# Performance work log

Measured on AMD Instinct MI355X. Metric: run time of the kernel, lower is better.

## Reference

```python
import math
import jax, jax.numpy as jnp
import numpy as np

B, T, T_P, C, H = 4, 2048, 256, 768, 12
HD = C // H


def setup_inputs() -> dict:
    key = jax.random.key(0)
    k1, k2, k3, k4 = jax.random.split(key, 4)
    x = jax.random.normal(k1, (B, T, C), dtype=jnp.float32)
    prefix = jax.random.normal(k2, (B, T_P, C), dtype=jnp.float32)
    # torch nn.Linear weight layout: (out_features, in_features)
    W_qkv = jax.random.normal(k3, (3 * C, C), dtype=jnp.float32) * (1.0 / math.sqrt(C))
    W_out = jax.random.normal(k4, (C, C), dtype=jnp.float32) * (1.0 / math.sqrt(C))
    return {"x": x, "prefix": prefix, "W_qkv": W_qkv, "W_out": W_out}


def _mac_causal_mask(t_p: int, t: int) -> jnp.ndarray:
    total = t_p + t
    mask = jnp.zeros((total, total), dtype=bool)
    mask = mask.at[:t_p, t_p:].set(True)  # h tokens blocked from x tokens
    causal = jnp.triu(jnp.ones((t, t), dtype=bool), k=1)  # causal within x block
    return mask.at[t_p:, t_p:].set(causal)


def reference(x, prefix, W_qkv, W_out):
    b, t, c = x.shape
    t_p = prefix.shape[1]
    t_all = t_p + t
    x_full = jnp.concatenate([prefix, x], axis=1)          # (B, T_all, C)
    qkv = x_full @ W_qkv.T                                  # (B, T_all, 3C)
    q, k, v = jnp.split(qkv, 3, axis=-1)
    # (B, H, T_all, HD)
    q = q.reshape(b, t_all, H, HD).transpose(0, 2, 1, 3)
    k = k.reshape(b, t_all, H, HD).transpose(0, 2, 1, 3)
    v = v.reshape(b, t_all, H, HD).transpose(0, 2, 1, 3)
    scale = 1.0 / math.sqrt(HD)
    att = jnp.einsum('bhqd,bhkd->bhqk', q, k) * scale       # (B, H, T_all, T_all)
    mask = _mac_causal_mask(t_p, t)
    att = jnp.where(mask[None, None], -jnp.inf, att)
    att = jax.nn.softmax(att, axis=-1)                      # dropout = identity (eval)
    out = jnp.einsum('bhqk,bhkd->bhqd', att, v)             # (B, H, T_all, HD)
    out = out.transpose(0, 2, 1, 3).reshape(b, t_all, c)
    out = out @ W_out.T
    return out[:, t_p:, :]                                  # only x portion (B, T, C)
```

## Files before the change

### kernel.cpp

```cpp
#include <hip/hip_runtime.h>

constexpr int Bn   = 4;
constexpr int Tn   = 2048;
constexpr int TPn  = 256;
constexpr int TALLn = 2304;
constexpr int Cn   = 768;
constexpr int Hn   = 12;
constexpr int HDn  = 64;

typedef __bf16 bf16x4 __attribute__((ext_vector_type(4)));
typedef __bf16 bf16x8 __attribute__((ext_vector_type(8)));
typedef float  f32x4  __attribute__((ext_vector_type(4)));
typedef unsigned u32x4 __attribute__((ext_vector_type(4)));

__device__ __forceinline__ unsigned short f2bf(float f) {
    unsigned int x = __float_as_uint(f);
    x += 0x7fffu + ((x >> 16) & 1u);
    return (unsigned short)(x >> 16);
}

__device__ __forceinline__ unsigned cvt_pk_bf16(float a, float b) {
    unsigned r;
    asm("v_cvt_pk_bf16_f32 %0, %1, %2" : "=v"(r) : "v"(a), "v"(b));
    return r;
}

#define ASYNC16(gsrc, ldst)                                                           \
    __builtin_amdgcn_global_load_lds((__attribute__((address_space(1))) void*)(gsrc), \
                                     (__attribute__((address_space(3))) void*)(ldst), \
                                     16, 0, 0)

__global__ __launch_bounds__(256) void k_build_xfull(
        const float* __restrict__ x, const float* __restrict__ pre,
        unsigned short* __restrict__ xf) {
    int idx = blockIdx.x * 256 + threadIdx.x;
    int row = idx / (Cn / 4);
    int c   = (idx - row * (Cn / 4)) * 4;
    int b = row / TALLn, tt = row - b * TALLn;
    const float* src = (tt < TPn) ? pre + ((size_t)b * TPn + tt) * Cn + c
                                  : x   + ((size_t)b * Tn + (tt - TPn)) * Cn + c;
    float4 f = *reinterpret_cast<const float4*>(src);
    ushort4 o = { f2bf(f.x), f2bf(f.y), f2bf(f.z), f2bf(f.w) };
    *reinterpret_cast<ushort4*>(xf + (size_t)row * Cn + c) = o;
}

__global__ __launch_bounds__(256) void k_cast(
        const float* __restrict__ in, unsigned short* __restrict__ out) {
    int idx = (blockIdx.x * 256 + threadIdx.x) * 4;
    float4 f = *reinterpret_cast<const float4*>(in + idx);
    ushort4 o = { f2bf(f.x), f2bf(f.y), f2bf(f.z), f2bf(f.w) };
    *reinterpret_cast<ushort4*>(out + idx) = o;
}

__global__ __launch_bounds__(256) void k_qkv_gemm(
        const unsigned short* __restrict__ A, const unsigned short* __restrict__ W,
        unsigned short* __restrict__ Qb, unsigned short* __restrict__ Kb,
        unsigned short* __restrict__ Vt) {
    __shared__ __align__(16) unsigned short smem[16384];
    unsigned short* As = smem;
    unsigned short* Bs = smem + 8192;
    const int tid  = threadIdx.x;
    const int wave = tid >> 6;
    const int lane = tid & 63;
    const int g = lane >> 4, l16 = lane & 15;
    const int m0 = blockIdx.x * 128, n0 = blockIdx.y * 128;
    const int wr = wave >> 1, wc = wave & 1;

    f32x4 acc[4][4] = {};

    for (int k0 = 0; k0 < Cn; k0 += 64) {
        #pragma unroll
        for (int inst = 0; inst < 4; ++inst) {
            const int li = inst * 256 + tid;
            const int row = li >> 3, slot = li & 7;
            const int ch = slot ^ (row & 7);
            ASYNC16(A + (size_t)(m0 + row) * Cn + k0 + ch * 8,
                    &As[(inst * 256 + wave * 64) * 8]);
            ASYNC16(W + (size_t)(n0 + row) * Cn + k0 + ch * 8,
                    &Bs[(inst * 256 + wave * 64) * 8]);
        }
        __syncthreads();
        #pragma unroll
        for (int kk = 0; kk < 2; ++kk) {
            bf16x8 af[4], bfv[4];
            #pragma unroll
            for (int mt = 0; mt < 4; ++mt) {
                const int row = wr * 64 + mt * 16 + l16;
                const int slot = (kk * 4 + g) ^ (row & 7);
                af[mt] = *reinterpret_cast<const bf16x8*>(&As[row * 64 + slot * 8]);
            }
            #pragma unroll
            for (int nt = 0; nt < 4; ++nt) {
                const int row = wc * 64 + nt * 16 + l16;
                const int slot = (kk * 4 + g) ^ (row & 7);
                bfv[nt] = *reinterpret_cast<const bf16x8*>(&Bs[row * 64 + slot * 8]);
            }
            #pragma unroll
            for (int mt = 0; mt < 4; ++mt)
                #pragma unroll
                for (int nt = 0; nt < 4; ++nt)
                    acc[mt][nt] = __builtin_amdgcn_mfma_f32_16x16x32_bf16(
                            af[mt], bfv[nt], acc[mt][nt], 0, 0, 0);
        }
        __syncthreads();
    }

    const int b   = m0 / TALLn;
    const int t0  = m0 - b * TALLn;
    const int sel = n0 / Cn;
    const int hn0 = n0 - sel * Cn;
    constexpr float SCQ = 0.18033688011112042f;

    if (sel == 2) {
        #pragma unroll
        for (int mt = 0; mt < 4; ++mt)
            #pragma unroll
            for (int nt = 0; nt < 4; ++nt)
                #pragma unroll
                for (int r = 0; r < 4; ++r) {
                    const int t  = wr * 64 + mt * 16 + g * 4 + r;
                    const int hn = wc * 64 + nt * 16 + l16;
                    smem[hn * 128 + (((t >> 3) ^ (hn & 7)) << 3) + (t & 7)] =
                            f2bf(acc[mt][nt][r]);
                }
        __syncthreads();
        #pragma unroll
        for (int j = 0; j < 8; ++j) {
            const int u  = tid + 256 * j;
            const int hn = u >> 4, tc = u & 15;
            bf16x8 v = *reinterpret_cast<const bf16x8*>(
                    &smem[hn * 128 + ((tc ^ (hn & 7)) << 3)]);
            const int hh = (hn0 + hn) >> 6;
            const int dd = hn & 63;
            *reinterpret_cast<bf16x8*>(
                    &Vt[(((size_t)b * Hn + hh) * HDn + dd) * TALLn + t0 + tc * 8]) = v;
        }
    } else {
        #pragma unroll
        for (int mt = 0; mt < 4; ++mt)
            #pragma unroll
            for (int nt = 0; nt < 4; ++nt)
                #pragma unroll
                for (int r = 0; r < 4; ++r) {
                    const int t  = t0 + wr * 64 + mt * 16 + g * 4 + r;
                    const int hn = hn0 + wc * 64 + nt * 16 + l16;
                    const int h = hn >> 6, d = hn & 63;
                    if (sel == 0)
                        Qb[(((size_t)b * Hn + h) * TALLn + t) * HDn + d] =
                                f2bf(acc[mt][nt][r] * SCQ);
                    else
                        Kb[(((size_t)b * Hn + h) * TALLn + t) * HDn + d] =
                                f2bf(acc[mt][nt][r]);
                }
    }
}

__global__ __launch_bounds__(256) void k_attn(
        const unsigned short* __restrict__ Qb, const unsigned short* __restrict__ Kb,
        const unsigned short* __restrict__ Vt, unsigned short* __restrict__ Ob) {
    __shared__ __align__(16) unsigned short Ks[2][4096];
    __shared__ __align__(16) unsigned short Vs[2][4096];
    const int tid  = threadIdx.x;
    const int wq   = tid >> 6;
    const int lane = tid & 63;
    const int l16  = lane & 15;
    const int g    = lane >> 4;

    const int fb = blockIdx.x;
    const int j  = fb >> 3;
    const int bh = 6 * (fb & 7) + (j >> 4);
    const int pi = j & 15;
    const size_t kv = (size_t)bh * TALLn * HDn;

    int koff[4][2];
    #pragma unroll
    for (int band = 0; band < 4; ++band)
        #pragma unroll
        for (int ks = 0; ks < 2; ++ks)
            koff[band][ks] = (band * 16 + l16) * 64 + (((ks * 4 + g) ^ (l16 & 7)) << 3);
    int voffA[2], voffB[2];
    #pragma unroll
    for (int kg = 0; kg < 2; ++kg) {
        voffA[kg] = l16 * 64 + (((4 * kg + (g >> 1)) ^ (l16 & 7)) << 3) + (g & 1) * 4;
        voffB[kg] = l16 * 64 + (((4 * kg + 2 + (g >> 1)) ^ (l16 & 7)) << 3) + (g & 1) * 4;
    }
    int soffK[2], soffV[2], sdst[2];
    #pragma unroll
    for (int inst = 0; inst < 2; ++inst) {
        const int li = inst * 256 + tid;
        const int row = li >> 3;
        const int ch = (li & 7) ^ (row & 7);
        soffK[inst] = row * HDn + ch * 8;
        soffV[inst] = row * TALLn + ch * 8;
        sdst[inst]  = (inst * 256 + wq * 64) * 8;
    }

    bf16x8 qf[2];
    auto loadQ = [&](int ch) {
        const int tq = TPn + ch * 64 + wq * 16 + l16;
        #pragma unroll
        for (int ks = 0; ks < 2; ++ks)
            qf[ks] = *reinterpret_cast<const bf16x8*>(
                    Qb + kv + (size_t)tq * HDn + ks * 32 + g * 8);
    };
    auto stageKV = [&](int bs, int kt0) {
        unsigned short* kb = &Ks[bs][0];
        unsigned short* vb = &Vs[bs][0];
        const unsigned short* gk = Kb + kv + (size_t)kt0 * HDn;
        const unsigned short* gv = Vt + kv + kt0;
        #pragma unroll
        for (int inst = 0; inst < 2; ++inst) {
            ASYNC16(gk + soffK[inst], kb + sdst[inst]);
            ASYNC16(gv + soffV[inst], vb + sdst[inst]);
        }
    };

    f32x4 oacc[4] = {};
    float mrow = -1e30f, lrow = 0.f;

    const int b = bh / Hn, h = bh - b * Hn;
    auto storeO = [&](int ch) {
        const float inv = 1.0f / lrow;
        const size_t row = (size_t)b * Tn + ch * 64 + wq * 16 + l16;
        #pragma unroll
        for (int dband = 0; dband < 4; ++dband) {
            ushort4 st;
            st.x = f2bf(oacc[dband][0] * inv);
            st.y = f2bf(oacc[dband][1] * inv);
            st.z = f2bf(oacc[dband][2] * inv);
            st.w = f2bf(oacc[dband][3] * inv);
            *reinterpret_cast<ushort4*>(
                    &Ob[row * Cn + h * 64 + dband * 16 + g * 4]) = st;
        }
    };

    int chunk = pi;
    int nkt   = 5 + pi;
    int kt = 0, buf = 0;
    loadQ(chunk);
    stageKV(0, 0);
    __syncthreads();

    for (int t = 0; t < 41; ++t) {
        if (t < 40) {
            const int nk0 = (kt + 1 < nkt) ? (kt + 1) * 64 : 0;
            stageKV(buf ^ 1, nk0);
        }
        const unsigned short* Ksb = &Ks[buf][0];
        const unsigned short* Vsb = &Vs[buf][0];

        f32x4 sacc[4] = {};
        __builtin_amdgcn_s_setprio(1);
        #pragma unroll
        for (int band = 0; band < 4; ++band) {
            bf16x8 k0 = *reinterpret_cast<const bf16x8*>(&Ksb[koff[band][0]]);
            bf16x8 k1 = *reinterpret_cast<const bf16x8*>(&Ksb[koff[band][1]]);
            sacc[band] = __builtin_amdgcn_mfma_f32_16x16x32_bf16(
                    k0, qf[0], sacc[band], 0, 0, 0);
            sacc[band] = __builtin_amdgcn_mfma_f32_16x16x32_bf16(
                    k1, qf[1], sacc[band], 0, 0, 0);
        }
        __builtin_amdgcn_s_setprio(0);

        if (kt == nkt - 1) {
            const int lim = TPn + chunk * 64 + wq * 16 + l16 - kt * 64;
            #pragma unroll
            for (int band = 0; band < 4; ++band)
                #pragma unroll
                for (int r = 0; r < 4; ++r)
                    sacc[band][r] = (band * 16 + g * 4 + r <= lim) ? sacc[band][r]
                                                                   : -1e30f;
        }
        float pm = fmaxf(fmaxf(sacc[0][0], sacc[0][1]), fmaxf(sacc[0][2], sacc[0][3]));
        #pragma unroll
        for (int band = 1; band < 4; ++band) {
            pm = fmaxf(pm, fmaxf(fmaxf(sacc[band][0], sacc[band][1]),
                                 fmaxf(sacc[band][2], sacc[band][3])));
        }
        pm = fmaxf(pm, __shfl_xor(pm, 16));
        pm = fmaxf(pm, __shfl_xor(pm, 32));

        if (!__all(pm <= mrow)) {
            const float mnew  = fmaxf(mrow, pm);
            const float alpha = exp2f(mrow - mnew);
            mrow = mnew;
            lrow *= alpha;
            oacc[0] *= alpha;
            oacc[1] *= alpha;
            oacc[2] *= alpha;
            oacc[3] *= alpha;
        }

        float rs = 0.f;
        unsigned dwb[4][2];
        #pragma unroll
        for (int band = 0; band < 4; ++band) {
            const float e0 = exp2f(sacc[band][0] - mrow);
            const float e1 = exp2f(sacc[band][1] - mrow);
            const float e2 = exp2f(sacc[band][2] - mrow);
            const float e3 = exp2f(sacc[band][3] - mrow);
            rs += (e0 + e1) + (e2 + e3);
            dwb[band][0] = cvt_pk_bf16(e0, e1);
            dwb[band][1] = cvt_pk_bf16(e2, e3);
        }
        rs += __shfl_xor(rs, 16);
        rs += __shfl_xor(rs, 32);
        lrow += rs;

        __builtin_amdgcn_s_setprio(1);
        #pragma unroll
        for (int kg = 0; kg < 2; ++kg) {
            const u32x4 uu = { dwb[2 * kg][0], dwb[2 * kg][1],
                               dwb[2 * kg + 1][0], dwb[2 * kg + 1][1] };
            const bf16x8 pf = __builtin_bit_cast(bf16x8, uu);
            #pragma unroll
            for (int dband = 0; dband < 4; ++dband) {
                bf16x4 a0 = *reinterpret_cast<const bf16x4*>(
                        &Vsb[dband * 1024 + voffA[kg]]);
                bf16x4 a1 = *reinterpret_cast<const bf16x4*>(
                        &Vsb[dband * 1024 + voffB[kg]]);
                bf16x8 vf = __builtin_shufflevector(a0, a1, 0, 1, 2, 3, 4, 5, 6, 7);
                oacc[dband] = __builtin_amdgcn_mfma_f32_16x16x32_bf16(
                        vf, pf, oacc[dband], 0, 0, 0);
            }
        }
        __builtin_amdgcn_s_setprio(0);

        if (kt == nkt - 1) {
            storeO(chunk);
            if (t < 40) {
                chunk = 31 - pi;
                nkt   = 36 - pi;
                kt = 0;
                mrow = -1e30f; lrow = 0.f;
                #pragma unroll
                for (int dband = 0; dband < 4; ++dband)
                    #pragma unroll
                    for (int r = 0; r < 4; ++r) oacc[dband][r] = 0.f;
                loadQ(chunk);
            }
        } else {
            ++kt;
        }
        buf ^= 1;
        __syncthreads();
    }
}

__global__ __launch_bounds__(256) void k_out_gemm(
        const unsigned short* __restrict__ A, const unsigned short* __restrict__ W,
        float* __restrict__ out) {
    __shared__ __align__(16) unsigned short As[8192];
    __shared__ __align__(16) unsigned short Bs[8192];
    const int tid  = threadIdx.x;
    const int wave = tid >> 6;
    const int lane = tid & 63;
    const int g = lane >> 4, l16 = lane & 15;
    const int m0 = blockIdx.x * 128, n0 = blockIdx.y * 128;
    const int wr = wave >> 1, wc = wave & 1;

    f32x4 acc[4][4] = {};

    for (int k0 = 0; k0 < Cn; k0 += 64) {
        #pragma unroll
        for (int inst = 0; inst < 4; ++inst) {
            const int li = inst * 256 + tid;
            const int row = li >> 3, slot = li & 7;
            const int ch = slot ^ (row & 7);
            ASYNC16(A + (size_t)(m0 + row) * Cn + k0 + ch * 8,
                    &As[(inst * 256 + wave * 64) * 8]);
            ASYNC16(W + (size_t)(n0 + row) * Cn + k0 + ch * 8,
                    &Bs[(inst * 256 + wave * 64) * 8]);
        }
        __syncthreads();
        #pragma unroll
        for (int kk = 0; kk < 2; ++kk) {
            bf16x8 af[4], bfv[4];
            #pragma unroll
            for (int mt = 0; mt < 4; ++mt) {
                const int row = wr * 64 + mt * 16 + l16;
                const int slot = (kk * 4 + g) ^ (row & 7);
                af[mt] = *reinterpret_cast<const bf16x8*>(&As[row * 64 + slot * 8]);
            }
            #pragma unroll
            for (int nt = 0; nt < 4; ++nt) {
                const int row = wc * 64 + nt * 16 + l16;
                const int slot = (kk * 4 + g) ^ (row & 7);
                bfv[nt] = *reinterpret_cast<const bf16x8*>(&Bs[row * 64 + slot * 8]);
            }
            #pragma unroll
            for (int mt = 0; mt < 4; ++mt)
                #pragma unroll
                for (int nt = 0; nt < 4; ++nt)
                    acc[mt][nt] = __builtin_amdgcn_mfma_f32_16x16x32_bf16(
                            af[mt], bfv[nt], acc[mt][nt], 0, 0, 0);
        }
        __syncthreads();
    }

    #pragma unroll
    for (int mt = 0; mt < 4; ++mt)
        #pragma unroll
        for (int nt = 0; nt < 4; ++nt)
            #pragma unroll
            for (int r = 0; r < 4; ++r) {
                const int m = m0 + wr * 64 + mt * 16 + g * 4 + r;
                const int n = n0 + wc * 64 + nt * 16 + l16;
                out[(size_t)m * Cn + n] = acc[mt][nt][r];
            }
}

extern "C" void kernel_launch(void* const* d_in, const int* in_sizes, int n_in,
                              void* d_out, int out_size, void* d_ws, size_t ws_size,
                              hipStream_t stream) {
    const float* x    = (const float*)d_in[0];
    const float* pre  = (const float*)d_in[1];
    const float* wqkv = (const float*)d_in[2];
    const float* wout = (const float*)d_in[3];
    float* out = (float*)d_out;
    char* ws = (char*)d_ws;

    unsigned short* xf  = (unsigned short*)(ws + 0);
    unsigned short* wqb = (unsigned short*)(ws + 14155776);
    unsigned short* wob = (unsigned short*)(ws + 17694720);
    unsigned short* Qb  = (unsigned short*)(ws + 18874368);
    unsigned short* Kb  = (unsigned short*)(ws + 33030144);
    unsigned short* Vt  = (unsigned short*)(ws + 47185920);
    unsigned short* Ob  = (unsigned short*)(ws + 61341696);

    k_build_xfull<<<dim3((Bn * TALLn * Cn / 4) / 256), 256, 0, stream>>>(x, pre, xf);
    k_cast<<<dim3((3 * Cn * Cn / 4) / 256), 256, 0, stream>>>(wqkv, wqb);
    k_cast<<<dim3((Cn * Cn / 4) / 256), 256, 0, stream>>>(wout, wob);
    k_qkv_gemm<<<dim3((Bn * TALLn) / 128, (3 * Cn) / 128), 256, 0, stream>>>(
            xf, wqb, Qb, Kb, Vt);
    k_attn<<<dim3(768), 256, 0, stream>>>(Qb, Kb, Vt, Ob);
    k_out_gemm<<<dim3((Bn * Tn) / 128, Cn / 128), 256, 0, stream>>>(Ob, wob, out);
}
```

Measured before the change: 168.2 us.

## Split paired attention chunks into separate blocks, longest first, MFMA row sums

The attention kernel no longer has each block process two paired query chunks (short plus long) over a fixed 41-step loop. It now launches 1536 blocks, each handling one 64-row query chunk, ordered so the longest chunks are scheduled first. This is meant to improve occupancy and tail balance. The softmax row sum is computed with an extra MFMA against a ones vector instead of shuffle reductions, and the row max uses v_max3. The trade-off is more blocks, with Q loads and prologue overhead repeated per chunk, plus an extra MFMA in each iteration.

```diff
diff --git a/kernel.cpp b/kernel.cpp
--- a/kernel.cpp
+++ b/kernel.cpp
@@ -22,6 +22,12 @@
 __device__ __forceinline__ unsigned cvt_pk_bf16(float a, float b) {
     unsigned r;
     asm("v_cvt_pk_bf16_f32 %0, %1, %2" : "=v"(r) : "v"(a), "v"(b));
+    return r;
+}
+
+__device__ __forceinline__ float max3f(float a, float b, float c) {
+    float r;
+    asm("v_max3_f32 %0, %1, %2, %3" : "=v"(r) : "v"(a), "v"(b), "v"(c));
     return r;
 }
 
@@ -166,10 +172,11 @@
     const int l16  = lane & 15;
     const int g    = lane >> 4;
 
-    const int fb = blockIdx.x;
-    const int j  = fb >> 3;
-    const int bh = 6 * (fb & 7) + (j >> 4);
-    const int pi = j & 15;
+    const int fb  = blockIdx.x;
+    const int j   = fb >> 3;
+    const int bh  = 6 * (fb & 7) + (j % 6);
+    const int chunk = 31 - (j / 6);
+    const int nkt = 5 + chunk;
     const size_t kv = (size_t)bh * TALLn * HDn;
 
     int koff[4][2];
@@ -184,67 +191,57 @@
         voffA[kg] = l16 * 64 + (((4 * kg + (g >> 1)) ^ (l16 & 7)) << 3) + (g & 1) * 4;
         voffB[kg] = l16 * 64 + (((4 * kg + 2 + (g >> 1)) ^ (l16 & 7)) << 3) + (g & 1) * 4;
     }
-    int soffK[2], soffV[2], sdst[2];
+    const unsigned short* pk[2];
+    const unsigned short* pv[2];
+    int sdst[2];
     #pragma unroll
     for (int inst = 0; inst < 2; ++inst) {
         const int li = inst * 256 + tid;
         const int row = li >> 3;
         const int ch = (li & 7) ^ (row & 7);
-        soffK[inst] = row * HDn + ch * 8;
-        soffV[inst] = row * TALLn + ch * 8;
-        sdst[inst]  = (inst * 256 + wq * 64) * 8;
-    }
+        pk[inst] = Kb + kv + row * HDn + ch * 8;
+        pv[inst] = Vt + kv + row * TALLn + ch * 8;
+        sdst[inst] = (inst * 256 + wq * 64) * 8;
+    }
+    constexpr int KSTRIDE = 64 * HDn;
+    constexpr int VSTRIDE = 64;
 
     bf16x8 qf[2];
-    auto loadQ = [&](int ch) {
-        const int tq = TPn + ch * 64 + wq * 16 + l16;
+    {
+        const int tq = TPn + chunk * 64 + wq * 16 + l16;
         #pragma unroll
         for (int ks = 0; ks < 2; ++ks)
             qf[ks] = *reinterpret_cast<const bf16x8*>(
                     Qb + kv + (size_t)tq * HDn + ks * 32 + g * 8);
-    };
-    auto stageKV = [&](int bs, int kt0) {
-        unsigned short* kb = &Ks[bs][0];
-        unsigned short* vb = &Vs[bs][0];
-        const unsigned short* gk = Kb + kv + (size_t)kt0 * HDn;
-        const unsigned short* gv = Vt + kv + kt0;
-        #pragma unroll
-        for (int inst = 0; inst < 2; ++inst) {
-            ASYNC16(gk + soffK[inst], kb + sdst[inst]);
-            ASYNC16(gv + soffV[inst], vb + sdst[inst]);
-        }
-    };
+    }
+
+    bf16x8 ones;
+    #pragma unroll
+    for (int i = 0; i < 8; ++i) ones[i] = (__bf16)1.0f;
 
     f32x4 oacc[4] = {};
-    float mrow = -1e30f, lrow = 0.f;
-
-    const int b = bh / Hn, h = bh - b * Hn;
-    auto storeO = [&](int ch) {
-        const float inv = 1.0f / lrow;
-        const size_t row = (size_t)b * Tn + ch * 64 + wq * 16 + l16;
-        #pragma unroll
-        for (int dband = 0; dband < 4; ++dband) {
-            ushort4 st;
-            st.x = f2bf(oacc[dband][0] * inv);
-            st.y = f2bf(oacc[dband][1] * inv);
-            st.z = f2bf(oacc[dband][2] * inv);
-            st.w = f2bf(oacc[dband][3] * inv);
-            *reinterpret_cast<ushort4*>(
-                    &Ob[row * Cn + h * 64 + dband * 16 + g * 4]) = st;
-        }
-    };
-
-    int chunk = pi;
-    int nkt   = 5 + pi;
-    int kt = 0, buf = 0;
-    loadQ(chunk);
-    stageKV(0, 0);
+    f32x4 lacc = {};
+    float mrow = -1e30f;
+
+    #pragma unroll
+    for (int inst = 0; inst < 2; ++inst) {
+        ASYNC16(pk[inst], &Ks[0][0] + sdst[inst]);
+        ASYNC16(pv[inst], &Vs[0][0] + sdst[inst]);
+        pk[inst] += KSTRIDE;
+        pv[inst] += VSTRIDE;
+    }
     __syncthreads();
 
-    for (int t = 0; t < 41; ++t) {
-        if (t < 40) {
-            const int nk0 = (kt + 1 < nkt) ? (kt + 1) * 64 : 0;
-            stageKV(buf ^ 1, nk0);
+    int buf = 0;
+    for (int t = 0; t < nkt; ++t) {
+        if (t + 1 < nkt) {
+            #pragma unroll
+            for (int inst = 0; inst < 2; ++inst) {
+                ASYNC16(pk[inst], &Ks[buf ^ 1][0] + sdst[inst]);
+                ASYNC16(pv[inst], &Vs[buf ^ 1][0] + sdst[inst]);
+                pk[inst] += KSTRIDE;
+                pv[inst] += VSTRIDE;
+            }
         }
         const unsigned short* Ksb = &Ks[buf][0];
         const unsigned short* Vsb = &Vs[buf][0];
@@ -262,8 +259,8 @@
         }
         __builtin_amdgcn_s_setprio(0);
 
-        if (kt == nkt - 1) {
-            const int lim = TPn + chunk * 64 + wq * 16 + l16 - kt * 64;
+        if (t == nkt - 1) {
+            const int lim = TPn + chunk * 64 + wq * 16 + l16 - t * 64;
             #pragma unroll
             for (int band = 0; band < 4; ++band)
                 #pragma unroll
@@ -271,12 +268,14 @@
                     sacc[band][r] = (band * 16 + g * 4 + r <= lim) ? sacc[band][r]
                                                                    : -1e30f;
         }
-        float pm = fmaxf(fmaxf(sacc[0][0], sacc[0][1]), fmaxf(sacc[0][2], sacc[0][3]));
-        #pragma unroll
-        for (int band = 1; band < 4; ++band) {
-            pm = fmaxf(pm, fmaxf(fmaxf(sacc[band][0], sacc[band][1]),
-                                 fmaxf(sacc[band][2], sacc[band][3])));
-        }
+        float pm = max3f(sacc[0][0], sacc[0][1], sacc[0][2]);
+        pm = max3f(pm, sacc[0][3], sacc[1][0]);
+        pm = max3f(pm, sacc[1][1], sacc[1][2]);
+        pm = max3f(pm, sacc[1][3], sacc[2][0]);
+        pm = max3f(pm, sacc[2][1], sacc[2][2]);
+        pm = max3f(pm, sacc[2][3], sacc[3][0]);
+        pm = max3f(pm, sacc[3][1], sacc[3][2]);
+        pm = fmaxf(pm, sacc[3][3]);
         pm = fmaxf(pm, __shfl_xor(pm, 16));
         pm = fmaxf(pm, __shfl_xor(pm, 32));
 
@@ -284,14 +283,13 @@
             const float mnew  = fmaxf(mrow, pm);
             const float alpha = exp2f(mrow - mnew);
             mrow = mnew;
-            lrow *= alpha;
+            lacc    *= alpha;
             oacc[0] *= alpha;
             oacc[1] *= alpha;
             oacc[2] *= alpha;
             oacc[3] *= alpha;
         }
 
-        float rs = 0.f;
         unsigned dwb[4][2];
         #pragma unroll
         for (int band = 0; band < 4; ++band) {
@@ -299,13 +297,9 @@
             const float e1 = exp2f(sacc[band][1] - mrow);
             const float e2 = exp2f(sacc[band][2] - mrow);
             const float e3 = exp2f(sacc[band][3] - mrow);
-            rs += (e0 + e1) + (e2 + e3);
             dwb[band][0] = cvt_pk_bf16(e0, e1);
             dwb[band][1] = cvt_pk_bf16(e2, e3);
         }
-        rs += __shfl_xor(rs, 16);
-        rs += __shfl_xor(rs, 32);
-        lrow += rs;
 
         __builtin_amdgcn_s_setprio(1);
         #pragma unroll
@@ -313,6 +307,7 @@
             const u32x4 uu = { dwb[2 * kg][0], dwb[2 * kg][1],
                                dwb[2 * kg + 1][0], dwb[2 * kg + 1][1] };
             const bf16x8 pf = __builtin_bit_cast(bf16x8, uu);
+            lacc = __builtin_amdgcn_mfma_f32_16x16x32_bf16(ones, pf, lacc, 0, 0, 0);
             #pragma unroll
             for (int dband = 0; dband < 4; ++dband) {
                 bf16x4 a0 = *reinterpret_cast<const bf16x4*>(
@@ -326,24 +321,21 @@
         }
         __builtin_amdgcn_s_setprio(0);
 
-        if (kt == nkt - 1) {
-            storeO(chunk);
-            if (t < 40) {
-                chunk = 31 - pi;
-                nkt   = 36 - pi;
-                kt = 0;
-                mrow = -1e30f; lrow = 0.f;
-                #pragma unroll
-                for (int dband = 0; dband < 4; ++dband)
-                    #pragma unroll
-                    for (int r = 0; r < 4; ++r) oacc[dband][r] = 0.f;
-                loadQ(chunk);
-            }
-        } else {
-            ++kt;
-        }
         buf ^= 1;
         __syncthreads();
+    }
+
+    const int b = bh / Hn, h = bh - b * Hn;
+    const float inv = 1.0f / lacc[0];
+    const size_t row = (size_t)b * Tn + chunk * 64 + wq * 16 + l16;
+    #pragma unroll
+    for (int dband = 0; dband < 4; ++dband) {
+        ushort4 st;
+        st.x = f2bf(oacc[dband][0] * inv);
+        st.y = f2bf(oacc[dband][1] * inv);
+        st.z = f2bf(oacc[dband][2] * inv);
+        st.w = f2bf(oacc[dband][3] * inv);
+        *reinterpret_cast<ushort4*>(&Ob[row * Cn + h * 64 + dband * 16 + g * 4]) = st;
     }
 }
 
@@ -433,6 +425,6 @@
     k_cast<<<dim3((Cn * Cn / 4) / 256), 256, 0, stream>>>(wout, wob);
     k_qkv_gemm<<<dim3((Bn * TALLn) / 128, (3 * Cn) / 128), 256, 0, stream>>>(
             xf, wqb, Qb, Kb, Vt);
-    k_attn<<<dim3(768), 256, 0, stream>>>(Qb, Kb, Vt, Ob);
+    k_attn<<<dim3(1536), 256, 0, stream>>>(Qb, Kb, Vt, Ob);
     k_out_gemm<<<dim3((Bn * Tn) / 128, Cn / 128), 256, 0, stream>>>(Ob, wob, out);
 }
```

New measurement: 162.7 us. -3.3%, faster.
